# Kernel tuning notes

Measured on AMD Instinct MI355X. Metric: run time of the kernel, lower is better.

The kernel has to match this reference:

```python
import jax, jax.numpy as jnp
import numpy as np

# GeoTempScheduler default: init_temp=0.1, gamma=0.9, patience=1; at step 0 -> temp = 0.1
TEMP = 0.1

R, K, D, DLOW, B = 8, 10, 256, 10, 4096


def setup_inputs() -> dict:
    key = jax.random.key(0)
    k1, k2 = jax.random.split(key)
    x = jax.random.normal(k1, (B, D), dtype=jnp.float32)
    # reset_parameters: Us ~ N(0, 0.1/sqrt(D))
    Us = jax.random.normal(k2, (R, K, D, DLOW), dtype=jnp.float32) * (0.1 / np.sqrt(D))
    return {"x": x, "Us": Us}


def reference(x, Us):
    # encode: project data onto each (replicate, cluster) subspace basis
    # z: (r, k, B, d)
    z = jnp.einsum('bD,rkDd->rkbd', x, Us)
    # decode: x_ = z @ Us^T  -> (r, k, B, D)
    x_ = jnp.einsum('rkbd,rkDd->rkbD', z, Us)
    # l2-squared reconstruction loss, (r, k, B) -> permuted to (B, r, k)
    loss = 0.5 * jnp.sum((x_ - x) ** 2, axis=-1)
    assign_obj = jnp.transpose(loss, (2, 0, 1))  # (B, r, k)
    # set_assign uses detached objective (loss.data): temperature-scaled soft assignment
    c = jax.nn.softmax(-jax.lax.stop_gradient(assign_obj) / TEMP, axis=2)  # (B, r, k)
    # x_ * c.permute(1,2,0).unsqueeze(3), summed over clusters -> (r, B, D)
    out = jnp.einsum('rkbD,brk->rbD', x_, c)
    return out
```

## Files before the change

### kernel.cpp

```cpp
#include <hip/hip_runtime.h>
#include <math.h>

typedef unsigned short ushort_t;
typedef unsigned int uint32_tt;
typedef __attribute__((ext_vector_type(8))) short bf16x8;
typedef __attribute__((ext_vector_type(4))) float f32x4;

#define NR   8
#define NK   10
#define ND   256
#define NDL  10
#define NB   4096
#define NN   100
#define NP   128
#define NP2  128

#define WS_GP   0
#define WS_XB   32768
#define WS_U1   (32768 + 2097152)
#define WS_U2   (WS_U1 + 524288)
#define WS_NEED (WS_U2 + 524288)

#define L_US   0
#define L_ZB   34816
#define L_GP   60416
#define L_SIZE 64416

__device__ __forceinline__ ushort_t f2bf(float f) {
    uint32_tt u = __float_as_uint(f);
    u = (u + 0x7FFF + ((u >> 16) & 1)) >> 16;
    return (ushort_t)u;
}

__global__ __launch_bounds__(256) void prep_kernel(const float* __restrict__ x,
                                                   const float* __restrict__ Us,
                                                   char* __restrict__ ws) {
    __shared__ float lu[ND * NDL];
    const int bid = blockIdx.x, tid = threadIdx.x;

    if (bid >= 80) {
        ushort_t* xb = (ushort_t*)(ws + WS_XB);
        const int base = (bid - 80) * 1024;
        #pragma unroll
        for (int v = 0; v < 4; ++v) {
            int i = base + v * 256 + tid;
            float4 vv = ((const float4*)x)[i];
            uint32_tt p0 = (uint32_tt)f2bf(vv.x) | ((uint32_tt)f2bf(vv.y) << 16);
            uint32_tt p1 = (uint32_tt)f2bf(vv.z) | ((uint32_tt)f2bf(vv.w) << 16);
            ((uint2*)xb)[i] = make_uint2(p0, p1);
        }
        return;
    }

    const int rk = bid;
    const int r  = rk / NK, k = rk - r * NK;
    const float* U = Us + (size_t)rk * ND * NDL;
    for (int i = tid; i < 640; i += 256)
        ((float4*)lu)[i] = ((const float4*)U)[i];
    __syncthreads();

    float* Gp = (float*)(ws + WS_GP);
    if (tid < NDL * NDL) {
        int d1 = tid / NDL, d2 = tid - d1 * NDL;
        float acc = 0.f;
        #pragma unroll 8
        for (int Di = 0; Di < ND; ++Di)
            acc += lu[Di * NDL + d1] * lu[Di * NDL + d2];
        Gp[(size_t)rk * 100 + tid] = (d1 == d2 ? 10.0f : 0.0f) - 5.0f * acc;
    }

    ushort_t* u1 = (ushort_t*)(ws + WS_U1);
    for (int p = tid; p < ND * NDL; p += 256) {
        int d = p >> 8, D = p & 255;
        u1[((size_t)r * NP + k * NDL + d) * ND + D] = f2bf(lu[D * NDL + d]);
    }

    ushort_t* u2 = (ushort_t*)(ws + WS_U2);
    {
        int D = tid;
        uint32_tt* dst = (uint32_tt*)(u2 + ((size_t)r * ND + D) * NP2 + k * NDL);
        const float* src = lu + D * NDL;
        #pragma unroll
        for (int j = 0; j < 5; ++j)
            dst[j] = (uint32_tt)f2bf(src[2 * j]) | ((uint32_tt)f2bf(src[2 * j + 1]) << 16);
    }

    if (k == NK - 1) {
        for (int p = tid; p < 28 * ND; p += 256) {
            int n = p >> 8, D = p & 255;
            u1[((size_t)r * NP + 100 + n) * ND + D] = 0;
        }
        uint32_tt* u2u = (uint32_tt*)u2;
        #pragma unroll
        for (int j = 0; j < 14; ++j)
            u2u[((size_t)r * ND + tid) * (NP2 / 2) + 50 + j] = 0;
    }
}

__global__ __launch_bounds__(256, 2) void ksub_mfma10(const char* __restrict__ ws,
                                                      float* __restrict__ out) {
    __shared__ __align__(16) char smem[L_SIZE];
    char*  usb = smem + L_US;
    float* gp  = (float*)(smem + L_GP);

    const int tid  = threadIdx.x;
    const int w    = tid >> 6;
    const int lane = tid & 63;
    const int c    = lane & 15;
    const int q    = lane >> 4;
    const int bid  = blockIdx.x;
    const int r    = bid & 7;
    const int bt   = bid >> 3;
    const int b0   = bt * 64;
    const int wb   = w & 1;
    const int pair = w >> 1;
    const int bloc = wb * 16 + c;

    const ushort_t* xbp = (const ushort_t*)(ws + WS_XB) + (size_t)(b0 + bloc) * ND + q * 8;
    const ushort_t* u1b = (const ushort_t*)(ws + WS_U1) + (size_t)r * NP * ND;
    const ushort_t* u2b = (const ushort_t*)(ws + WS_U2) + (size_t)r * ND * NP2;
    const float*    gpg = (const float*)(ws + WS_GP) + (size_t)r * 1000;

    for (int i = tid; i < 1000; i += 256) gp[i] = gpg[i];

    f32x4 acc1[2][4];
    #pragma unroll
    for (int t2 = 0; t2 < 2; ++t2)
        #pragma unroll
        for (int tt = 0; tt < 4; ++tt) acc1[t2][tt] = (f32x4){0.f, 0.f, 0.f, 0.f};

    #pragma unroll 1
    for (int h = 0; h < 2; ++h) {
        {
            const ushort_t* src = u1b + h * 128;
            #pragma unroll
            for (int j = 0; j < 8; ++j) {
                int cid = tid + j * 256;
                int n = cid >> 4, m = cid & 15;
                bf16x8 v = *(const bf16x8*)(src + (size_t)n * ND + m * 8);
                *(bf16x8*)(usb + n * 272 + m * 16) = v;
            }
        }
        bf16x8 xf[2][4];
        #pragma unroll
        for (int tile = 0; tile < 2; ++tile)
            #pragma unroll
            for (int d = 0; d < 4; ++d)
                xf[tile][d] = *(const bf16x8*)(xbp + (size_t)tile * 32 * ND + (h * 4 + d) * 32);
        __syncthreads();

        #pragma unroll
        for (int tt = 0; tt < 4; ++tt) {
            const int t = pair * 4 + tt;
            #pragma unroll
            for (int d = 0; d < 4; ++d) {
                bf16x8 uf = *(const bf16x8*)(usb + (t * 16 + c) * 272 + d * 64 + q * 16);
                acc1[0][tt] = __builtin_amdgcn_mfma_f32_16x16x32_bf16(uf, xf[0][d], acc1[0][tt], 0, 0, 0);
                acc1[1][tt] = __builtin_amdgcn_mfma_f32_16x16x32_bf16(uf, xf[1][d], acc1[1][tt], 0, 0, 0);
            }
        }
        __syncthreads();
    }

    #pragma unroll
    for (int tile = 0; tile < 2; ++tile) {
        float* zb = (float*)(smem + L_ZB + tile * 12800);
        #pragma unroll
        for (int tt = 0; tt < 4; ++tt) {
            int t = pair * 4 + tt;
            #pragma unroll
            for (int rg = 0; rg < 4; ++rg) {
                int n = t * 16 + q * 4 + rg;
                if (n < NN) zb[bloc * 100 + n] = acc1[tile][tt][rg];
            }
        }
    }
    __syncthreads();

    const int bsm = tid >> 3;
    const int kq  = tid & 7;
    #pragma unroll 1
    for (int tile = 0; tile < 2; ++tile) {
        float*    zb = (float*)(smem + L_ZB + tile * 12800);
        ushort_t* wt = (ushort_t*)(smem + L_ZB + tile * 8704);
        float zk[2][10], ee[2];
        {
            const float* zr = zb + bsm * 100;
            float L[2];
            #pragma unroll
            for (int jj = 0; jj < 2; ++jj) {
                int k = kq + 8 * jj;
                L[jj] = -1e30f;
                if (k < NK) {
                    #pragma unroll
                    for (int d = 0; d < 10; ++d) zk[jj][d] = zr[k * 10 + d];
                    const float* g = gp + k * 100;
                    float acc = 0.f;
                    #pragma unroll
                    for (int d1 = 0; d1 < 10; ++d1) {
                        float t2 = 0.f;
                        #pragma unroll
                        for (int d2 = 0; d2 < 10; ++d2) t2 += g[d1 * 10 + d2] * zk[jj][d2];
                        acc += t2 * zk[jj][d1];
                    }
                    L[jj] = acc;
                }
            }
            float m = fmaxf(L[0], L[1]);
            m = fmaxf(m, __shfl_xor(m, 1));
            m = fmaxf(m, __shfl_xor(m, 2));
            m = fmaxf(m, __shfl_xor(m, 4));
            float s = 0.f;
            #pragma unroll
            for (int jj = 0; jj < 2; ++jj) {
                ee[jj] = (kq + 8 * jj < NK) ? __expf(L[jj] - m) : 0.f;
                s += ee[jj];
            }
            s += __shfl_xor(s, 1);
            s += __shfl_xor(s, 2);
            s += __shfl_xor(s, 4);
            float inv = 1.0f / s;
            #pragma unroll
            for (int jj = 0; jj < 2; ++jj) ee[jj] *= inv;
        }
        __syncthreads();

        #pragma unroll
        for (int jj = 0; jj < 2; ++jj) {
            int k = kq + 8 * jj;
            if (k < NK) {
                #pragma unroll
                for (int d = 0; d < 10; ++d)
                    wt[bsm * 136 + k * 10 + d] = f2bf(ee[jj] * zk[jj][d]);
            }
        }
        {
            int row = tid >> 4, p = tid & 15;
            if (row < 32 && p < 14) ((uint32_tt*)wt)[row * 68 + 50 + p] = 0;
            row = (tid + 256) >> 4;
            if (row < 32 && p < 14) ((uint32_tt*)wt)[row * 68 + 50 + p] = 0;
        }
    }
    __syncthreads();

    const ushort_t* wt0 = (ushort_t*)(smem + L_ZB);
    const ushort_t* wt1 = (ushort_t*)(smem + L_ZB + 8704);
    const size_t orow = (size_t)r * NB + b0;

    #pragma unroll 1
    for (int h = 0; h < 2; ++h) {
        {
            const ushort_t* src = u2b + (size_t)h * 128 * NP2;
            #pragma unroll
            for (int j = 0; j < 8; ++j) {
                int cid = tid + j * 256;
                int n = cid >> 4, m = cid & 15;
                bf16x8 v = *(const bf16x8*)(src + (size_t)n * NP2 + m * 8);
                *(bf16x8*)(usb + n * 272 + m * 16) = v;
            }
        }
        __syncthreads();

        f32x4 acc3[2][4];
        #pragma unroll
        for (int t2 = 0; t2 < 2; ++t2)
            #pragma unroll
            for (int jj = 0; jj < 4; ++jj) acc3[t2][jj] = (f32x4){0.f, 0.f, 0.f, 0.f};

        #pragma unroll
        for (int nc = 0; nc < 4; ++nc) {
            bf16x8 bf0 = *(const bf16x8*)(wt0 + bloc * 136 + nc * 32 + q * 8);
            bf16x8 bf1 = *(const bf16x8*)(wt1 + bloc * 136 + nc * 32 + q * 8);
            #pragma unroll
            for (int jj = 0; jj < 4; ++jj) {
                bf16x8 af = *(const bf16x8*)(usb + (pair * 64 + jj * 16 + c) * 272 + nc * 64 + q * 16);
                acc3[0][jj] = __builtin_amdgcn_mfma_f32_16x16x32_bf16(af, bf0, acc3[0][jj], 0, 0, 0);
                acc3[1][jj] = __builtin_amdgcn_mfma_f32_16x16x32_bf16(af, bf1, acc3[1][jj], 0, 0, 0);
            }
        }

        #pragma unroll
        for (int tile = 0; tile < 2; ++tile)
            #pragma unroll
            for (int jj = 0; jj < 4; ++jj)
                __builtin_nontemporal_store(acc3[tile][jj],
                    (f32x4*)(out + (orow + tile * 32 + bloc) * ND + h * 128 + pair * 64 + jj * 16 + q * 4));
        __syncthreads();
    }
}

#define XS_S 68
#define US_S 132
#define ZB_S 104
#define WT_S 68
#define U2_S 68
#define OFF_WT 0
#define OFF_SH 6800
#define OFF_GP 13600
#define SMEM_F 14600

__global__ __launch_bounds__(128) void gram_kernel(const float* __restrict__ Us,
                                                   float* __restrict__ Gp) {
    int rk = blockIdx.x;
    const float* U = Us + (size_t)rk * ND * NDL;
    __shared__ float u[ND * NDL];
    for (int i = threadIdx.x; i < ND * NDL; i += blockDim.x) u[i] = U[i];
    __syncthreads();
    int e = threadIdx.x;
    if (e < NDL * NDL) {
        int d1 = e / NDL, d2 = e % NDL;
        float acc = 0.f;
        #pragma unroll 8
        for (int Di = 0; Di < ND; ++Di)
            acc += u[Di * NDL + d1] * u[Di * NDL + d2];
        Gp[(size_t)rk * (NDL * NDL) + e] = (d1 == d2 ? 10.0f : 0.0f) - 5.0f * acc;
    }
}

__global__ __launch_bounds__(256, 2) void ksub_fused(const float* __restrict__ x,
                                                     const float* __restrict__ Us,
                                                     const float* __restrict__ Gp,
                                                     float* __restrict__ out) {
    __shared__ float smemf[SMEM_F];
    float* wT   = smemf + OFF_WT;
    float* xsf  = smemf + OFF_SH;
    float* usf  = smemf + OFF_SH + 2176;
    float* zbuf = smemf + OFF_SH;
    float* u2   = smemf + OFF_SH;
    float* gp   = smemf + OFF_GP;

    const int tid = threadIdx.x;
    const int r   = blockIdx.y;
    const int b0  = blockIdx.x * 64;

    for (int i = tid; i < NK * NDL * NDL; i += 256)
        gp[i] = Gp[(size_t)r * (NK * NDL * NDL) + i];

    const int nt = tid & 15;
    const int bt = tid >> 4;
    float acc[4][8];
    #pragma unroll
    for (int j = 0; j < 4; ++j)
        #pragma unroll
        for (int i = 0; i < 8; ++i) acc[j][i] = 0.f;

    for (int cch = 0; cch < 8; ++cch) {
        __syncthreads();
        for (int i = tid; i < 512; i += 256) {
            int b = i >> 3, f = i & 7;
            float4 v = ((const float4*)(x + (size_t)(b0 + b) * ND))[cch * 8 + f];
            float* dst = xsf + (f * 4) * XS_S + b;
            dst[0] = v.x; dst[XS_S] = v.y; dst[2 * XS_S] = v.z; dst[3 * XS_S] = v.w;
        }
        for (int p = tid; p < 320; p += 256) {
            int k = p >> 5, Dl = p & 31;
            const float* g = Us + ((size_t)((r * NK + k) * ND) + cch * 32 + Dl) * NDL;
            float* dst = usf + Dl * US_S + k * NDL;
            #pragma unroll
            for (int d = 0; d < 10; ++d) dst[d] = g[d];
        }
        __syncthreads();
        #pragma unroll 4
        for (int Dl = 0; Dl < 32; ++Dl) {
            float4 xv = *(const float4*)(xsf + Dl * XS_S + bt * 4);
            float4 ua = *(const float4*)(usf + Dl * US_S + nt * 8);
            float4 ub = *(const float4*)(usf + Dl * US_S + nt * 8 + 4);
            float xa[4] = {xv.x, xv.y, xv.z, xv.w};
            float uu[8] = {ua.x, ua.y, ua.z, ua.w, ub.x, ub.y, ub.z, ub.w};
            #pragma unroll
            for (int j = 0; j < 4; ++j)
                #pragma unroll
                for (int i = 0; i < 8; ++i) acc[j][i] += xa[j] * uu[i];
        }
    }
    __syncthreads();
    if (nt < 12) {
        #pragma unroll
        for (int j = 0; j < 4; ++j) {
            float* zp = zbuf + (bt * 4 + j) * ZB_S + nt * 8;
            *(float4*)(zp)     = make_float4(acc[j][0], acc[j][1], acc[j][2], acc[j][3]);
            *(float4*)(zp + 4) = make_float4(acc[j][4], acc[j][5], acc[j][6], acc[j][7]);
        }
    } else if (nt == 12) {
        #pragma unroll
        for (int j = 0; j < 4; ++j) {
            float* zp = zbuf + (bt * 4 + j) * ZB_S + 96;
            *(float4*)(zp) = make_float4(acc[j][0], acc[j][1], acc[j][2], acc[j][3]);
        }
    }
    __syncthreads();
    if (tid < 64) {
        const int b_l = tid;
        const float* zrow = zbuf + b_l * ZB_S;
        float L[10];
        #pragma unroll
        for (int k = 0; k < NK; ++k) {
            float zkk[10];
            #pragma unroll
            for (int d = 0; d < 10; ++d) zkk[d] = zrow[k * 10 + d];
            const float* g = gp + k * 100;
            float a2 = 0.f;
            #pragma unroll
            for (int d1 = 0; d1 < 10; ++d1) {
                float t = 0.f;
                #pragma unroll
                for (int d2 = 0; d2 < 10; ++d2) t += g[d1 * 10 + d2] * zkk[d2];
                a2 += t * zkk[d1];
            }
            L[k] = a2;
        }
        float m = L[0];
        #pragma unroll
        for (int k = 1; k < NK; ++k) m = fmaxf(m, L[k]);
        float e[10], s = 0.f;
        #pragma unroll
        for (int k = 0; k < NK; ++k) { e[k] = __expf(L[k] - m); s += e[k]; }
        float inv = 1.0f / s;
        #pragma unroll
        for (int k = 0; k < NK; ++k) {
            float ck = e[k] * inv;
            #pragma unroll
            for (int d = 0; d < 10; ++d)
                wT[(k * 10 + d) * WT_S + b_l] = ck * zrow[k * 10 + d];
        }
    }
    const int Dt  = tid & 15;
    const int bt2 = tid >> 4;
    for (int c2 = 0; c2 < 4; ++c2) {
        __syncthreads();
        for (int p = tid; p < 640; p += 256) {
            int k = p >> 6, Dl = p & 63;
            const float* g = Us + ((size_t)((r * NK + k) * ND) + c2 * 64 + Dl) * NDL;
            float* dst = u2 + (k * NDL) * U2_S + Dl;
            #pragma unroll
            for (int d = 0; d < 10; ++d) dst[d * U2_S] = g[d];
        }
        __syncthreads();
        float o[4][4];
        #pragma unroll
        for (int j = 0; j < 4; ++j)
            #pragma unroll
            for (int i = 0; i < 4; ++i) o[j][i] = 0.f;
        #pragma unroll 4
        for (int n = 0; n < NN; ++n) {
            float4 wv = *(const float4*)(wT + n * WT_S + bt2 * 4);
            float4 uv = *(const float4*)(u2 + n * U2_S + Dt * 4);
            float wa[4] = {wv.x, wv.y, wv.z, wv.w};
            float ub[4] = {uv.x, uv.y, uv.z, uv.w};
            #pragma unroll
            for (int j = 0; j < 4; ++j)
                #pragma unroll
                for (int i = 0; i < 4; ++i) o[j][i] += wa[j] * ub[i];
        }
        #pragma unroll
        for (int j = 0; j < 4; ++j) {
            float* op = out + ((size_t)r * NB + b0 + bt2 * 4 + j) * ND + c2 * 64 + Dt * 4;
            *(float4*)op = make_float4(o[j][0], o[j][1], o[j][2], o[j][3]);
        }
    }
}

extern "C" void kernel_launch(void* const* d_in, const int* in_sizes, int n_in,
                              void* d_out, int out_size, void* d_ws, size_t ws_size,
                              hipStream_t stream) {
    const float* x  = (const float*)d_in[0];
    const float* Us = (const float*)d_in[1];
    float* out = (float*)d_out;

    if (ws_size >= (size_t)WS_NEED) {
        prep_kernel<<<dim3(336), 256, 0, stream>>>(x, Us, (char*)d_ws);
        ksub_mfma10<<<dim3(512), 256, 0, stream>>>((const char*)d_ws, out);
    } else {
        gram_kernel<<<dim3(NR * NK), 128, 0, stream>>>(Us, (float*)d_ws);
        ksub_fused<<<dim3(NB / 64, NR), 256, 0, stream>>>(x, Us, (float*)d_ws, out);
    }
}
```

Before: 89.30 us.

## Fuse prep and main kernels with flag-based inter-block synchronization

```diff
diff --git a/kernel.cpp b/kernel.cpp
--- a/kernel.cpp
+++ b/kernel.cpp
@@ -15,11 +15,11 @@
 #define NP   128
 #define NP2  128
 
-#define WS_GP   0
-#define WS_XB   32768
-#define WS_U1   (32768 + 2097152)
-#define WS_U2   (WS_U1 + 524288)
-#define WS_NEED (WS_U2 + 524288)
+#define WS_GP    0
+#define WS_U1    32768
+#define WS_U2    (32768 + 524288)
+#define WS_FLAGS (WS_U2 + 524288)
+#define WS_NEED  (WS_FLAGS + 320)
 
 #define L_US   0
 #define L_ZB   34816
@@ -32,28 +32,13 @@
     return (ushort_t)u;
 }
 
-__global__ __launch_bounds__(256) void prep_kernel(const float* __restrict__ x,
-                                                   const float* __restrict__ Us,
-                                                   char* __restrict__ ws) {
-    __shared__ float lu[ND * NDL];
-    const int bid = blockIdx.x, tid = threadIdx.x;
-
-    if (bid >= 80) {
-        ushort_t* xb = (ushort_t*)(ws + WS_XB);
-        const int base = (bid - 80) * 1024;
-        #pragma unroll
-        for (int v = 0; v < 4; ++v) {
-            int i = base + v * 256 + tid;
-            float4 vv = ((const float4*)x)[i];
-            uint32_tt p0 = (uint32_tt)f2bf(vv.x) | ((uint32_tt)f2bf(vv.y) << 16);
-            uint32_tt p1 = (uint32_tt)f2bf(vv.z) | ((uint32_tt)f2bf(vv.w) << 16);
-            ((uint2*)xb)[i] = make_uint2(p0, p1);
-        }
-        return;
-    }
-
-    const int rk = bid;
-    const int r  = rk / NK, k = rk - r * NK;
+__device__ __forceinline__ uint32_tt rk_magic(int rk) {
+    return 0x9E3779B9u * (uint32_tt)(rk + 1) ^ 0x5CA1AB1Eu;
+}
+
+__device__ __forceinline__ void prep_rk(int rk, int tid, const float* __restrict__ Us,
+                                        char* __restrict__ ws, float* lu) {
+    const int r = rk / NK, k = rk - r * NK;
     const float* U = Us + (size_t)rk * ND * NDL;
     for (int i = tid; i < 640; i += 256)
         ((float4*)lu)[i] = ((const float4*)U)[i];
@@ -97,26 +82,53 @@
     }
 }
 
-__global__ __launch_bounds__(256, 2) void ksub_mfma10(const char* __restrict__ ws,
-                                                      float* __restrict__ out) {
+__global__ __launch_bounds__(256, 2) void fused_all(const float* __restrict__ x,
+                                                    const float* __restrict__ Us,
+                                                    char* __restrict__ ws,
+                                                    float* __restrict__ out) {
     __shared__ __align__(16) char smem[L_SIZE];
+    const int tid = threadIdx.x;
+    const int bid = blockIdx.x;
+    uint32_tt* flg = (uint32_tt*)(ws + WS_FLAGS);
+
+    if (bid < 80) {
+        prep_rk(bid, tid, Us, ws, (float*)smem);
+        __syncthreads();
+        if (tid == 0) {
+            __threadfence();
+            __hip_atomic_store(&flg[bid], rk_magic(bid),
+                               __ATOMIC_RELEASE, __HIP_MEMORY_SCOPE_AGENT);
+        }
+    }
+
+    const int r = bid & 7;
+
+    if (tid < 10) {
+        const int rk = r * 10 + tid;
+        const uint32_tt want = rk_magic(rk);
+        int guard = 0;
+        while (__hip_atomic_load(&flg[rk], __ATOMIC_ACQUIRE,
+                                 __HIP_MEMORY_SCOPE_AGENT) != want) {
+            __builtin_amdgcn_s_sleep(2);
+            if (++guard > (1 << 24)) break;
+        }
+    }
+    __syncthreads();
+
     char*  usb = smem + L_US;
     float* gp  = (float*)(smem + L_GP);
 
-    const int tid  = threadIdx.x;
     const int w    = tid >> 6;
     const int lane = tid & 63;
     const int c    = lane & 15;
     const int q    = lane >> 4;
-    const int bid  = blockIdx.x;
-    const int r    = bid & 7;
     const int bt   = bid >> 3;
     const int b0   = bt * 64;
     const int wb   = w & 1;
     const int pair = w >> 1;
     const int bloc = wb * 16 + c;
 
-    const ushort_t* xbp = (const ushort_t*)(ws + WS_XB) + (size_t)(b0 + bloc) * ND + q * 8;
+    const float*    xg  = x + (size_t)(b0 + bloc) * ND + q * 8;
     const ushort_t* u1b = (const ushort_t*)(ws + WS_U1) + (size_t)r * NP * ND;
     const ushort_t* u2b = (const ushort_t*)(ws + WS_U2) + (size_t)r * ND * NP2;
     const float*    gpg = (const float*)(ws + WS_GP) + (size_t)r * 1000;
@@ -143,10 +155,20 @@
         }
         bf16x8 xf[2][4];
         #pragma unroll
-        for (int tile = 0; tile < 2; ++tile)
-            #pragma unroll
-            for (int d = 0; d < 4; ++d)
-                xf[tile][d] = *(const bf16x8*)(xbp + (size_t)tile * 32 * ND + (h * 4 + d) * 32);
+        for (int tile = 0; tile < 2; ++tile) {
+            #pragma unroll
+            for (int d = 0; d < 4; ++d) {
+                const float* p = xg + (size_t)tile * 32 * ND + (h * 4 + d) * 32;
+                float4 a = *(const float4*)p;
+                float4 b = *(const float4*)(p + 4);
+                bf16x8 v;
+                v[0] = (short)f2bf(a.x); v[1] = (short)f2bf(a.y);
+                v[2] = (short)f2bf(a.z); v[3] = (short)f2bf(a.w);
+                v[4] = (short)f2bf(b.x); v[5] = (short)f2bf(b.y);
+                v[6] = (short)f2bf(b.z); v[7] = (short)f2bf(b.w);
+                xf[tile][d] = v;
+            }
+        }
         __syncthreads();
 
         #pragma unroll
@@ -468,8 +490,7 @@
     float* out = (float*)d_out;
 
     if (ws_size >= (size_t)WS_NEED) {
-        prep_kernel<<<dim3(336), 256, 0, stream>>>(x, Us, (char*)d_ws);
-        ksub_mfma10<<<dim3(512), 256, 0, stream>>>((const char*)d_ws, out);
+        fused_all<<<dim3(512), 256, 0, stream>>>(x, Us, (char*)d_ws, out);
     } else {
         gram_kernel<<<dim3(NR * NK), 128, 0, stream>>>(Us, (float*)d_ws);
         ksub_fused<<<dim3(NB / 64, NR), 256, 0, stream>>>(x, Us, (float*)d_ws, out);
```

Measured after the change: 132.2 us. +48.1%, slower.

## Register-prefetch next Us stage during MFMA and remap block-to-replicate order

Applied to the files above, without the earlier changes.

```diff
diff --git a/kernel.cpp b/kernel.cpp
--- a/kernel.cpp
+++ b/kernel.cpp
@@ -97,7 +97,7 @@
     }
 }
 
-__global__ __launch_bounds__(256, 2) void ksub_mfma10(const char* __restrict__ ws,
+__global__ __launch_bounds__(256, 2) void ksub_mfma11(const char* __restrict__ ws,
                                                       float* __restrict__ out) {
     __shared__ __align__(16) char smem[L_SIZE];
     char*  usb = smem + L_US;
@@ -109,8 +109,8 @@
     const int c    = lane & 15;
     const int q    = lane >> 4;
     const int bid  = blockIdx.x;
-    const int r    = bid & 7;
-    const int bt   = bid >> 3;
+    const int r    = bid >> 6;
+    const int bt   = bid & 63;
     const int b0   = bt * 64;
     const int wb   = w & 1;
     const int pair = w >> 1;
@@ -123,43 +123,72 @@
 
     for (int i = tid; i < 1000; i += 256) gp[i] = gpg[i];
 
+    bf16x8 sA[8], sB[8];
+
+    const int sn0 = tid >> 4;
+    const int sm  = tid & 15;
+
+    #pragma unroll
+    for (int j = 0; j < 8; ++j)
+        sA[j] = *(const bf16x8*)(u1b + (size_t)(sn0 + j * 16) * ND + sm * 8);
+
+    bf16x8 xf[2][4];
+    #pragma unroll
+    for (int tile = 0; tile < 2; ++tile)
+        #pragma unroll
+        for (int d = 0; d < 4; ++d)
+            xf[tile][d] = *(const bf16x8*)(xbp + (size_t)tile * 32 * ND + d * 32);
+
+    #pragma unroll
+    for (int j = 0; j < 8; ++j)
+        *(bf16x8*)(usb + (sn0 + j * 16) * 272 + sm * 16) = sA[j];
+    __syncthreads();
+
+    #pragma unroll
+    for (int j = 0; j < 8; ++j)
+        sB[j] = *(const bf16x8*)(u1b + 128 + (size_t)(sn0 + j * 16) * ND + sm * 8);
+
     f32x4 acc1[2][4];
     #pragma unroll
     for (int t2 = 0; t2 < 2; ++t2)
         #pragma unroll
         for (int tt = 0; tt < 4; ++tt) acc1[t2][tt] = (f32x4){0.f, 0.f, 0.f, 0.f};
 
-    #pragma unroll 1
-    for (int h = 0; h < 2; ++h) {
-        {
-            const ushort_t* src = u1b + h * 128;
-            #pragma unroll
-            for (int j = 0; j < 8; ++j) {
-                int cid = tid + j * 256;
-                int n = cid >> 4, m = cid & 15;
-                bf16x8 v = *(const bf16x8*)(src + (size_t)n * ND + m * 8);
-                *(bf16x8*)(usb + n * 272 + m * 16) = v;
-            }
-        }
-        bf16x8 xf[2][4];
-        #pragma unroll
-        for (int tile = 0; tile < 2; ++tile)
-            #pragma unroll
-            for (int d = 0; d < 4; ++d)
-                xf[tile][d] = *(const bf16x8*)(xbp + (size_t)tile * 32 * ND + (h * 4 + d) * 32);
-        __syncthreads();
-
-        #pragma unroll
-        for (int tt = 0; tt < 4; ++tt) {
-            const int t = pair * 4 + tt;
-            #pragma unroll
-            for (int d = 0; d < 4; ++d) {
-                bf16x8 uf = *(const bf16x8*)(usb + (t * 16 + c) * 272 + d * 64 + q * 16);
-                acc1[0][tt] = __builtin_amdgcn_mfma_f32_16x16x32_bf16(uf, xf[0][d], acc1[0][tt], 0, 0, 0);
-                acc1[1][tt] = __builtin_amdgcn_mfma_f32_16x16x32_bf16(uf, xf[1][d], acc1[1][tt], 0, 0, 0);
-            }
-        }
-        __syncthreads();
+    #pragma unroll
+    for (int tt = 0; tt < 4; ++tt) {
+        const int t = pair * 4 + tt;
+        #pragma unroll
+        for (int d = 0; d < 4; ++d) {
+            bf16x8 uf = *(const bf16x8*)(usb + (t * 16 + c) * 272 + d * 64 + q * 16);
+            acc1[0][tt] = __builtin_amdgcn_mfma_f32_16x16x32_bf16(uf, xf[0][d], acc1[0][tt], 0, 0, 0);
+            acc1[1][tt] = __builtin_amdgcn_mfma_f32_16x16x32_bf16(uf, xf[1][d], acc1[1][tt], 0, 0, 0);
+        }
+    }
+    __syncthreads();
+
+    #pragma unroll
+    for (int j = 0; j < 8; ++j)
+        *(bf16x8*)(usb + (sn0 + j * 16) * 272 + sm * 16) = sB[j];
+    #pragma unroll
+    for (int tile = 0; tile < 2; ++tile)
+        #pragma unroll
+        for (int d = 0; d < 4; ++d)
+            xf[tile][d] = *(const bf16x8*)(xbp + (size_t)tile * 32 * ND + (4 + d) * 32);
+    __syncthreads();
+
+    #pragma unroll
+    for (int j = 0; j < 8; ++j)
+        sA[j] = *(const bf16x8*)(u2b + (size_t)(sn0 + j * 16) * NP2 + sm * 8);
+
+    #pragma unroll
+    for (int tt = 0; tt < 4; ++tt) {
+        const int t = pair * 4 + tt;
+        #pragma unroll
+        for (int d = 0; d < 4; ++d) {
+            bf16x8 uf = *(const bf16x8*)(usb + (t * 16 + c) * 272 + d * 64 + q * 16);
+            acc1[0][tt] = __builtin_amdgcn_mfma_f32_16x16x32_bf16(uf, xf[0][d], acc1[0][tt], 0, 0, 0);
+            acc1[1][tt] = __builtin_amdgcn_mfma_f32_16x16x32_bf16(uf, xf[1][d], acc1[1][tt], 0, 0, 0);
+        }
     }
 
     #pragma unroll
@@ -176,6 +205,10 @@
         }
     }
     __syncthreads();
+
+    #pragma unroll
+    for (int j = 0; j < 8; ++j)
+        *(bf16x8*)(usb + (sn0 + j * 16) * 272 + sm * 16) = sA[j];
 
     const int bsm = tid >> 3;
     const int kq  = tid & 7;
@@ -247,20 +280,11 @@
     const ushort_t* wt1 = (ushort_t*)(smem + L_ZB + 8704);
     const size_t orow = (size_t)r * NB + b0;
 
-    #pragma unroll 1
-    for (int h = 0; h < 2; ++h) {
-        {
-            const ushort_t* src = u2b + (size_t)h * 128 * NP2;
-            #pragma unroll
-            for (int j = 0; j < 8; ++j) {
-                int cid = tid + j * 256;
-                int n = cid >> 4, m = cid & 15;
-                bf16x8 v = *(const bf16x8*)(src + (size_t)n * NP2 + m * 8);
-                *(bf16x8*)(usb + n * 272 + m * 16) = v;
-            }
-        }
-        __syncthreads();
-
+    #pragma unroll
+    for (int j = 0; j < 8; ++j)
+        sB[j] = *(const bf16x8*)(u2b + (size_t)(128 + sn0 + j * 16) * NP2 + sm * 8);
+
+    {
         f32x4 acc3[2][4];
         #pragma unroll
         for (int t2 = 0; t2 < 2; ++t2)
@@ -278,14 +302,44 @@
                 acc3[1][jj] = __builtin_amdgcn_mfma_f32_16x16x32_bf16(af, bf1, acc3[1][jj], 0, 0, 0);
             }
         }
-
         #pragma unroll
         for (int tile = 0; tile < 2; ++tile)
             #pragma unroll
             for (int jj = 0; jj < 4; ++jj)
                 __builtin_nontemporal_store(acc3[tile][jj],
-                    (f32x4*)(out + (orow + tile * 32 + bloc) * ND + h * 128 + pair * 64 + jj * 16 + q * 4));
-        __syncthreads();
+                    (f32x4*)(out + (orow + tile * 32 + bloc) * ND + pair * 64 + jj * 16 + q * 4));
+    }
+    __syncthreads();
+
+    #pragma unroll
+    for (int j = 0; j < 8; ++j)
+        *(bf16x8*)(usb + (sn0 + j * 16) * 272 + sm * 16) = sB[j];
+    __syncthreads();
+
+    {
+        f32x4 acc3[2][4];
+        #pragma unroll
+        for (int t2 = 0; t2 < 2; ++t2)
+            #pragma unroll
+            for (int jj = 0; jj < 4; ++jj) acc3[t2][jj] = (f32x4){0.f, 0.f, 0.f, 0.f};
+
+        #pragma unroll
+        for (int nc = 0; nc < 4; ++nc) {
+            bf16x8 bf0 = *(const bf16x8*)(wt0 + bloc * 136 + nc * 32 + q * 8);
+            bf16x8 bf1 = *(const bf16x8*)(wt1 + bloc * 136 + nc * 32 + q * 8);
+            #pragma unroll
+            for (int jj = 0; jj < 4; ++jj) {
+                bf16x8 af = *(const bf16x8*)(usb + (pair * 64 + jj * 16 + c) * 272 + nc * 64 + q * 16);
+                acc3[0][jj] = __builtin_amdgcn_mfma_f32_16x16x32_bf16(af, bf0, acc3[0][jj], 0, 0, 0);
+                acc3[1][jj] = __builtin_amdgcn_mfma_f32_16x16x32_bf16(af, bf1, acc3[1][jj], 0, 0, 0);
+            }
+        }
+        #pragma unroll
+        for (int tile = 0; tile < 2; ++tile)
+            #pragma unroll
+            for (int jj = 0; jj < 4; ++jj)
+                __builtin_nontemporal_store(acc3[tile][jj],
+                    (f32x4*)(out + (orow + tile * 32 + bloc) * ND + 128 + pair * 64 + jj * 16 + q * 4));
     }
 }
 
@@ -469,7 +523,7 @@
 
     if (ws_size >= (size_t)WS_NEED) {
         prep_kernel<<<dim3(336), 256, 0, stream>>>(x, Us, (char*)d_ws);
-        ksub_mfma10<<<dim3(512), 256, 0, stream>>>((const char*)d_ws, out);
+        ksub_mfma11<<<dim3(512), 256, 0, stream>>>((const char*)d_ws, out);
     } else {
         gram_kernel<<<dim3(NR * NK), 128, 0, stream>>>(Us, (float*)d_ws);
         ksub_fused<<<dim3(NB / 64, NR), 256, 0, stream>>>(x, Us, (float*)d_ws, out);
```

Measured after the change: 85.64 us (median of 2 runs). 1.04x faster.

## Use 512-thread blocks over 128 rows, staging full U1/U2 in LDS once

Applied to the files above, without the earlier changes.

```diff
diff --git a/kernel.cpp b/kernel.cpp
--- a/kernel.cpp
+++ b/kernel.cpp
@@ -22,9 +22,9 @@
 #define WS_NEED (WS_U2 + 524288)
 
 #define L_US   0
-#define L_ZB   34816
-#define L_GP   60416
-#define L_SIZE 64416
+#define L_ZB   69632
+#define L_GP   120832
+#define L_SIZE 124832
 
 __device__ __forceinline__ ushort_t f2bf(float f) {
     uint32_tt u = __float_as_uint(f);
@@ -97,8 +97,8 @@
     }
 }
 
-__global__ __launch_bounds__(256, 2) void ksub_mfma10(const char* __restrict__ ws,
-                                                      float* __restrict__ out) {
+__global__ __launch_bounds__(512, 1) void ksub_big(const char* __restrict__ ws,
+                                                   float* __restrict__ out) {
     __shared__ __align__(16) char smem[L_SIZE];
     char*  usb = smem + L_US;
     float* gp  = (float*)(smem + L_GP);
@@ -109,80 +109,80 @@
     const int c    = lane & 15;
     const int q    = lane >> 4;
     const int bid  = blockIdx.x;
-    const int r    = bid & 7;
-    const int bt   = bid >> 3;
-    const int b0   = bt * 64;
-    const int wb   = w & 1;
-    const int pair = w >> 1;
-    const int bloc = wb * 16 + c;
-
-    const ushort_t* xbp = (const ushort_t*)(ws + WS_XB) + (size_t)(b0 + bloc) * ND + q * 8;
+    const int r    = bid >> 5;
+    const int bt   = bid & 31;
+    const int b0   = bt * 128;
+    const int tile = w >> 1;
+    const int bloc = (w & 1) * 16 + c;
+
+    const ushort_t* xbp = (const ushort_t*)(ws + WS_XB)
+                          + (size_t)(b0 + tile * 32 + bloc) * ND + q * 8;
     const ushort_t* u1b = (const ushort_t*)(ws + WS_U1) + (size_t)r * NP * ND;
     const ushort_t* u2b = (const ushort_t*)(ws + WS_U2) + (size_t)r * ND * NP2;
     const float*    gpg = (const float*)(ws + WS_GP) + (size_t)r * 1000;
 
-    for (int i = tid; i < 1000; i += 256) gp[i] = gpg[i];
-
-    f32x4 acc1[2][4];
-    #pragma unroll
-    for (int t2 = 0; t2 < 2; ++t2)
-        #pragma unroll
-        for (int tt = 0; tt < 4; ++tt) acc1[t2][tt] = (f32x4){0.f, 0.f, 0.f, 0.f};
-
-    #pragma unroll 1
-    for (int h = 0; h < 2; ++h) {
-        {
-            const ushort_t* src = u1b + h * 128;
-            #pragma unroll
-            for (int j = 0; j < 8; ++j) {
-                int cid = tid + j * 256;
-                int n = cid >> 4, m = cid & 15;
-                bf16x8 v = *(const bf16x8*)(src + (size_t)n * ND + m * 8);
-                *(bf16x8*)(usb + n * 272 + m * 16) = v;
-            }
-        }
-        bf16x8 xf[2][4];
-        #pragma unroll
-        for (int tile = 0; tile < 2; ++tile)
-            #pragma unroll
-            for (int d = 0; d < 4; ++d)
-                xf[tile][d] = *(const bf16x8*)(xbp + (size_t)tile * 32 * ND + (h * 4 + d) * 32);
-        __syncthreads();
-
-        #pragma unroll
-        for (int tt = 0; tt < 4; ++tt) {
-            const int t = pair * 4 + tt;
-            #pragma unroll
-            for (int d = 0; d < 4; ++d) {
-                bf16x8 uf = *(const bf16x8*)(usb + (t * 16 + c) * 272 + d * 64 + q * 16);
-                acc1[0][tt] = __builtin_amdgcn_mfma_f32_16x16x32_bf16(uf, xf[0][d], acc1[0][tt], 0, 0, 0);
-                acc1[1][tt] = __builtin_amdgcn_mfma_f32_16x16x32_bf16(uf, xf[1][d], acc1[1][tt], 0, 0, 0);
-            }
-        }
-        __syncthreads();
-    }
-
-    #pragma unroll
-    for (int tile = 0; tile < 2; ++tile) {
+    for (int i = tid; i < 1000; i += 512) gp[i] = gpg[i];
+
+    {
+        const int n1 = tid >> 5, m1 = tid & 31;
+        bf16x8 sA[8];
+        #pragma unroll
+        for (int j = 0; j < 8; ++j)
+            sA[j] = *(const bf16x8*)(u1b + (size_t)(n1 + j * 16) * ND + m1 * 8);
+        #pragma unroll
+        for (int j = 0; j < 8; ++j)
+            *(bf16x8*)(usb + (n1 + j * 16) * 528 + m1 * 16) = sA[j];
+    }
+
+    bf16x8 xf[8];
+    #pragma unroll
+    for (int d = 0; d < 8; ++d)
+        xf[d] = *(const bf16x8*)(xbp + d * 32);
+    __syncthreads();
+
+    f32x4 acc1[8];
+    #pragma unroll
+    for (int t = 0; t < 8; ++t) acc1[t] = (f32x4){0.f, 0.f, 0.f, 0.f};
+
+    #pragma unroll
+    for (int d = 0; d < 8; ++d) {
+        #pragma unroll
+        for (int t = 0; t < 8; ++t) {
+            bf16x8 uf = *(const bf16x8*)(usb + (t * 16 + c) * 528 + d * 64 + q * 16);
+            acc1[t] = __builtin_amdgcn_mfma_f32_16x16x32_bf16(uf, xf[d], acc1[t], 0, 0, 0);
+        }
+    }
+
+    {
         float* zb = (float*)(smem + L_ZB + tile * 12800);
         #pragma unroll
-        for (int tt = 0; tt < 4; ++tt) {
-            int t = pair * 4 + tt;
+        for (int t = 0; t < 8; ++t) {
             #pragma unroll
             for (int rg = 0; rg < 4; ++rg) {
                 int n = t * 16 + q * 4 + rg;
-                if (n < NN) zb[bloc * 100 + n] = acc1[tile][tt][rg];
+                if (n < NN) zb[bloc * 100 + n] = acc1[t][rg];
             }
         }
     }
     __syncthreads();
 
-    const int bsm = tid >> 3;
-    const int kq  = tid & 7;
+    bf16x8 sB[8];
+    {
+        const int n2 = tid >> 4, m2 = tid & 15;
+        #pragma unroll
+        for (int j = 0; j < 8; ++j)
+            sB[j] = *(const bf16x8*)(u2b + (size_t)(n2 + j * 32) * NP2 + m2 * 8);
+    }
+
+    const int tid2  = tid & 255;
+    const int thalf = tid >> 8;
+    const int bsm   = tid2 >> 3;
+    const int kq    = tid2 & 7;
     #pragma unroll 1
-    for (int tile = 0; tile < 2; ++tile) {
-        float*    zb = (float*)(smem + L_ZB + tile * 12800);
-        ushort_t* wt = (ushort_t*)(smem + L_ZB + tile * 8704);
+    for (int pass = 0; pass < 2; ++pass) {
+        const int ti = pass * 2 + thalf;
+        float*    zb = (float*)(smem + L_ZB + ti * 12800);
+        ushort_t* wt = (ushort_t*)(smem + L_ZB + ti * 8704);
         float zk[2][10], ee[2];
         {
             const float* zr = zb + bsm * 100;
@@ -235,58 +235,42 @@
             }
         }
         {
-            int row = tid >> 4, p = tid & 15;
-            if (row < 32 && p < 14) ((uint32_tt*)wt)[row * 68 + 50 + p] = 0;
-            row = (tid + 256) >> 4;
-            if (row < 32 && p < 14) ((uint32_tt*)wt)[row * 68 + 50 + p] = 0;
-        }
-    }
-    __syncthreads();
-
-    const ushort_t* wt0 = (ushort_t*)(smem + L_ZB);
-    const ushort_t* wt1 = (ushort_t*)(smem + L_ZB + 8704);
-    const size_t orow = (size_t)r * NB + b0;
-
-    #pragma unroll 1
-    for (int h = 0; h < 2; ++h) {
-        {
-            const ushort_t* src = u2b + (size_t)h * 128 * NP2;
-            #pragma unroll
-            for (int j = 0; j < 8; ++j) {
-                int cid = tid + j * 256;
-                int n = cid >> 4, m = cid & 15;
-                bf16x8 v = *(const bf16x8*)(src + (size_t)n * NP2 + m * 8);
-                *(bf16x8*)(usb + n * 272 + m * 16) = v;
-            }
-        }
-        __syncthreads();
-
-        f32x4 acc3[2][4];
-        #pragma unroll
-        for (int t2 = 0; t2 < 2; ++t2)
-            #pragma unroll
-            for (int jj = 0; jj < 4; ++jj) acc3[t2][jj] = (f32x4){0.f, 0.f, 0.f, 0.f};
-
-        #pragma unroll
-        for (int nc = 0; nc < 4; ++nc) {
-            bf16x8 bf0 = *(const bf16x8*)(wt0 + bloc * 136 + nc * 32 + q * 8);
-            bf16x8 bf1 = *(const bf16x8*)(wt1 + bloc * 136 + nc * 32 + q * 8);
-            #pragma unroll
-            for (int jj = 0; jj < 4; ++jj) {
-                bf16x8 af = *(const bf16x8*)(usb + (pair * 64 + jj * 16 + c) * 272 + nc * 64 + q * 16);
-                acc3[0][jj] = __builtin_amdgcn_mfma_f32_16x16x32_bf16(af, bf0, acc3[0][jj], 0, 0, 0);
-                acc3[1][jj] = __builtin_amdgcn_mfma_f32_16x16x32_bf16(af, bf1, acc3[1][jj], 0, 0, 0);
-            }
-        }
-
-        #pragma unroll
-        for (int tile = 0; tile < 2; ++tile)
-            #pragma unroll
-            for (int jj = 0; jj < 4; ++jj)
-                __builtin_nontemporal_store(acc3[tile][jj],
-                    (f32x4*)(out + (orow + tile * 32 + bloc) * ND + h * 128 + pair * 64 + jj * 16 + q * 4));
-        __syncthreads();
-    }
+            int row = tid2 >> 4, p = tid2 & 15;
+            if (p < 14) ((uint32_tt*)wt)[row * 68 + 50 + p] = 0;
+            row = (tid2 + 256) >> 4;
+            if (p < 14) ((uint32_tt*)wt)[row * 68 + 50 + p] = 0;
+        }
+    }
+    __syncthreads();
+
+    {
+        const int n2 = tid >> 4, m2 = tid & 15;
+        #pragma unroll
+        for (int j = 0; j < 8; ++j)
+            *(bf16x8*)(usb + (n2 + j * 32) * 272 + m2 * 16) = sB[j];
+    }
+    __syncthreads();
+
+    const ushort_t* wtp = (const ushort_t*)(smem + L_ZB + tile * 8704);
+    f32x4 acc3[16];
+    #pragma unroll
+    for (int jj = 0; jj < 16; ++jj) acc3[jj] = (f32x4){0.f, 0.f, 0.f, 0.f};
+
+    #pragma unroll
+    for (int nc = 0; nc < 4; ++nc) {
+        bf16x8 bfr = *(const bf16x8*)(wtp + bloc * 136 + nc * 32 + q * 8);
+        #pragma unroll
+        for (int jj = 0; jj < 16; ++jj) {
+            bf16x8 af = *(const bf16x8*)(usb + (jj * 16 + c) * 272 + nc * 64 + q * 16);
+            acc3[jj] = __builtin_amdgcn_mfma_f32_16x16x32_bf16(af, bfr, acc3[jj], 0, 0, 0);
+        }
+    }
+
+    const size_t orow = (size_t)r * NB + b0 + tile * 32 + bloc;
+    #pragma unroll
+    for (int jj = 0; jj < 16; ++jj)
+        __builtin_nontemporal_store(acc3[jj],
+            (f32x4*)(out + orow * ND + jj * 16 + q * 4));
 }
 
 #define XS_S 68
@@ -469,7 +453,7 @@
 
     if (ws_size >= (size_t)WS_NEED) {
         prep_kernel<<<dim3(336), 256, 0, stream>>>(x, Us, (char*)d_ws);
-        ksub_mfma10<<<dim3(512), 256, 0, stream>>>((const char*)d_ws, out);
+        ksub_big<<<dim3(256), 512, 0, stream>>>((const char*)d_ws, out);
     } else {
         gram_kernel<<<dim3(NR * NK), 128, 0, stream>>>(Us, (float*)d_ws);
         ksub_fused<<<dim3(NB / 64, NR), 256, 0, stream>>>(x, Us, (float*)d_ws, out);
```

Result: no change. 89.70 us (+0.4%).
